# Kernel tuning notes

Hardware: AMD Instinct MI355X
Metric: run time of the kernel (lower is better)

The kernel has to match this reference:

```python
import jax, jax.numpy as jnp
import numpy as np

H_OUT, W_OUT = 473, 473  # original image size the logits are upsampled to
BN_EPS = 1e-5


def _conv(x, w, pad):
    return jax.lax.conv_general_dilated(
        x, w, window_strides=(1, 1), padding=[(pad, pad), (pad, pad)],
        dimension_numbers=('NCHW', 'OIHW', 'NCHW'))


def _bn(x, g, b):
    # BatchNorm2d in training mode: batch statistics over (N, H, W)
    m = jnp.mean(x, axis=(0, 2, 3), keepdims=True)
    v = jnp.var(x, axis=(0, 2, 3), keepdims=True)
    return (x - m) * jax.lax.rsqrt(v + BN_EPS) * g.reshape(1, -1, 1, 1) + b.reshape(1, -1, 1, 1)


def setup_inputs() -> dict:
    key = jax.random.key(0)
    ks = jax.random.split(key, 8)
    B, C, Hf, Wf, NC = 2, 256, 60, 60, 2
    return {
        'V_a': jax.random.normal(ks[0], (B, C, Hf, Wf), jnp.float32),
        'V_b': jax.random.normal(ks[1], (B, C, Hf, Wf), jnp.float32),
        'D_a': jax.random.normal(ks[2], (B, C, Hf, Wf), jnp.float32),
        'W_e': jax.random.normal(ks[3], (C, C), jnp.float32) * 0.02,
        'gate_w': jax.random.normal(ks[4], (1, C, 1, 1), jnp.float32) * 0.01,
        'conv1_w': jax.random.normal(ks[5], (C, 3 * C, 3, 3), jnp.float32) * 0.01,
        'conv2_w': jax.random.normal(ks[6], (C, 2 * C, 3, 3), jnp.float32) * 0.01,
        'bn1_g': jnp.ones((C,), jnp.float32),
        'bn1_b': jnp.zeros((C,), jnp.float32),
        'bn2_g': jnp.ones((C,), jnp.float32),
        'bn2_b': jnp.zeros((C,), jnp.float32),
        'cls1_w': jax.random.normal(ks[7], (NC, C, 1, 1), jnp.float32) * 0.01,
        'cls1_b': jnp.zeros((NC,), jnp.float32),
        'cls2_w': jax.random.normal(jax.random.fold_in(key, 9), (NC, C, 1, 1), jnp.float32) * 0.01,
        'cls2_b': jnp.zeros((NC,), jnp.float32),
    }


def reference(V_a, V_b, D_a, W_e, gate_w, conv1_w, conv2_w,
              bn1_g, bn1_b, bn2_g, bn2_b, cls1_w, cls1_b, cls2_w, cls2_b):
    B, C, Hf, Wf = V_a.shape
    N = Hf * Wf
    V_a_flat = V_a.reshape(B, C, N)
    V_b_flat = V_b.reshape(B, C, N)

    # linear_e on transposed A features, then affinity S = (A^T W^T) B
    weighted = jnp.einsum('bcn,dc->bnd', V_a_flat, W_e)        # [B, N, C]
    S = jnp.einsum('bnd,bdm->bnm', weighted, V_b_flat)         # [B, N, N]

    S_row = jax.nn.softmax(S, axis=1)                          # softmax over dim 1
    S_colT = jax.nn.softmax(jnp.swapaxes(S, 1, 2), axis=1)     # softmax of S^T over dim 1

    Z_b = jnp.einsum('bcn,bnm->bcm', V_a_flat, S_row)          # attended for view b
    Z_a = jnp.einsum('bcn,bnm->bcm', V_b_flat, S_colT)         # attended for view a

    att1 = Z_a.reshape(B, C, Hf, Wf)
    att2 = Z_b.reshape(B, C, Hf, Wf)

    # 1x1 sigmoid gates
    att1 = att1 * jax.nn.sigmoid(_conv(att1, gate_w, 0))
    att2 = att2 * jax.nn.sigmoid(_conv(att2, gate_w, 0))

    # conc1: branch-1 concatenates gated attention, RGB feat, and depth feat
    x1 = jnp.concatenate([att1, V_a, D_a], axis=1)             # [B, 3C, Hf, Wf]
    x2 = jnp.concatenate([att2, V_b], axis=1)                  # [B, 2C, Hf, Wf]

    x1 = jax.nn.relu(_bn(_conv(x1, conv1_w, 1), bn1_g, bn1_b))
    x2 = jax.nn.relu(_bn(_conv(x2, conv2_w, 1), bn2_g, bn2_b))

    x1 = _conv(x1, cls1_w, 0) + cls1_b.reshape(1, -1, 1, 1)
    x2 = _conv(x2, cls2_w, 0) + cls2_b.reshape(1, -1, 1, 1)

    NC = cls1_w.shape[0]
    x1 = jax.image.resize(x1, (B, NC, H_OUT, W_OUT), 'linear')
    x2 = jax.image.resize(x2, (B, NC, H_OUT, W_OUT), 'linear')
    return jax.nn.sigmoid(x1), jax.nn.sigmoid(x2)
```

## Files before the change

### kernel.cpp

```cpp
#include <hip/hip_runtime.h>

#define BB 2
#define CC 256
#define NN 3600
#define NCH 2
#define HO 473
#define WO 473
#define NP 3648
#define NR 3712
#define NTI 29
#define ZKS 6
#define CZKS 3

typedef unsigned short u16;
typedef __attribute__((ext_vector_type(8))) short short8;
typedef __attribute__((ext_vector_type(4))) float f32x4;

static __device__ __forceinline__ u16 f2bf(float f) {
    unsigned u = __float_as_uint(f);
    unsigned r = (u + 0x7FFF + ((u >> 16) & 1)) >> 16;
    return (u16)r;
}
static __device__ __forceinline__ u16 f2h(float f) {
    _Float16 h = (_Float16)f;
    return __builtin_bit_cast(unsigned short, h);
}
static __device__ __forceinline__ float h2f(u16 u) {
    _Float16 h = __builtin_bit_cast(_Float16, u);
    return (float)h;
}

static __device__ __forceinline__ void glds16(const u16* g, u16* l) {
    __builtin_amdgcn_global_load_lds(
        (const __attribute__((address_space(1))) void*)g,
        (__attribute__((address_space(3))) void*)l, 16, 0, 0);
}


__global__ __launch_bounds__(256)
void gemm_we(const u16* __restrict__ vat, const u16* __restrict__ web,
             u16* __restrict__ wgtb)
{
    __shared__ u16 As[128 * 64];
    __shared__ u16 Bs[128 * 64];
    const u16* A = vat + (long)blockIdx.z * NR * CC;
    u16* Cp = wgtb + (long)blockIdx.z * NR * CC;

    const int t = threadIdx.x;
    const int w = t >> 6, lane = t & 63;
    const int mh = (w >> 1) * 64, nh = (w & 1) * 64;
    const int lm = lane & 15, quad = lane >> 4;
    const int m0 = blockIdx.y * 128, n0 = blockIdx.x * 128;
    const int wb = t & 192;

    f32x4 acc[4][4] = {};

    for (int k0 = 0; k0 < CC; k0 += 64) {
#pragma unroll
        for (int i = 0; i < 4; ++i) {
            int idx = i * 256 + t;
            int row = idx >> 3;
            int sc8 = ((idx ^ row) & 7) * 8;
            glds16(A + (long)(m0 + row) * CC + k0 + sc8, &As[(i * 256 + wb) * 8]);
            glds16(web + (long)(n0 + row) * CC + k0 + sc8, &Bs[(i * 256 + wb) * 8]);
        }
        __syncthreads();
#pragma unroll
        for (int s = 0; s < 2; ++s) {
            short8 a[4], b[4];
#pragma unroll
            for (int i = 0; i < 4; ++i)
                a[i] = *(const short8*)(&As[(mh + i * 16 + lm) * 64 + ((s * 4 + quad) ^ (lm & 7)) * 8]);
#pragma unroll
            for (int j = 0; j < 4; ++j)
                b[j] = *(const short8*)(&Bs[(nh + j * 16 + lm) * 64 + ((s * 4 + quad) ^ (lm & 7)) * 8]);
#pragma unroll
            for (int i = 0; i < 4; ++i)
#pragma unroll
                for (int j = 0; j < 4; ++j)
                    acc[i][j] = __builtin_amdgcn_mfma_f32_16x16x32_bf16(a[i], b[j], acc[i][j], 0, 0, 0);
        }
        __syncthreads();
    }
#pragma unroll
    for (int i = 0; i < 4; ++i)
#pragma unroll
        for (int r = 0; r < 4; ++r) {
            int row = m0 + mh + i * 16 + quad * 4 + r;
            if (row < NN)
#pragma unroll
                for (int j = 0; j < 4; ++j) {
                    int col = n0 + nh + j * 16 + lm;
                    if (col < CC) Cp[(long)row * CC + col] = f2bf(acc[i][j][r]);
                }
        }
}

__global__ __launch_bounds__(256)
void gemm_s_stats(const u16* __restrict__ A, const u16* __restrict__ B,
                  u16* __restrict__ Sh, u16* __restrict__ STh,
                  float* __restrict__ prowm, float* __restrict__ prows,
                  float* __restrict__ pcolm, float* __restrict__ pcols)
{
    __shared__ u16 smem[17408];
    u16* As = smem;
    u16* Bs = smem + 8192;

    const int t = threadIdx.x;
    const int w = t >> 6, lane = t & 63;
    const int mh = (w >> 1) * 64, nh = (w & 1) * 64;
    const int lm = lane & 15, quad = lane >> 4;
    const int m0 = blockIdx.y * 128, n0 = blockIdx.x * 128;
    const int wb = t & 192;

    f32x4 acc[4][4] = {};

    for (int k0 = 0; k0 < CC; k0 += 64) {
#pragma unroll
        for (int i = 0; i < 4; ++i) {
            int idx = i * 256 + t;
            int row = idx >> 3;
            int sc8 = ((idx ^ row) & 7) * 8;
            glds16(A + (long)(m0 + row) * CC + k0 + sc8, &As[(i * 256 + wb) * 8]);
            glds16(B + (long)(n0 + row) * CC + k0 + sc8, &Bs[(i * 256 + wb) * 8]);
        }
        __syncthreads();
#pragma unroll
        for (int s = 0; s < 2; ++s) {
            short8 a[4], b[4];
#pragma unroll
            for (int i = 0; i < 4; ++i)
                a[i] = *(const short8*)(&As[(mh + i * 16 + lm) * 64 + ((s * 4 + quad) ^ (lm & 7)) * 8]);
#pragma unroll
            for (int j = 0; j < 4; ++j)
                b[j] = *(const short8*)(&Bs[(nh + j * 16 + lm) * 64 + ((s * 4 + quad) ^ (lm & 7)) * 8]);
#pragma unroll
            for (int i = 0; i < 4; ++i)
#pragma unroll
                for (int j = 0; j < 4; ++j)
                    acc[i][j] = __builtin_amdgcn_mfma_f32_16x16x32_bf16(a[i], b[j], acc[i][j], 0, 0, 0);
        }
        __syncthreads();
    }

    u16* tr = smem;

#pragma unroll
    for (int i = 0; i < 4; ++i)
#pragma unroll
        for (int j = 0; j < 4; ++j)
#pragma unroll
            for (int r = 0; r < 4; ++r)
                tr[(mh + i * 16 + quad * 4 + r) * 136 + (nh + j * 16 + lm)] = f2h(acc[i][j][r]);
    __syncthreads();
    {
        int row = t >> 1, hf = t & 1;
        int ng = m0 + row;
        if (ng < NN) {
#pragma unroll
            for (int q = 0; q < 8; ++q) {
                int cb = n0 + hf * 64 + q * 8;
                if (cb < NN)
                    *(uint4*)(&Sh[(long)ng * NP + cb]) =
                        *(const uint4*)(&tr[row * 136 + hf * 64 + q * 8]);
            }
        }
    }
    __syncthreads();

    bool cval[4];
#pragma unroll
    for (int j = 0; j < 4; ++j) cval[j] = (n0 + nh + j * 16 + lm) < NN;

    float* sm = (float*)smem;
    float* rowm = sm;
    float* rows_ = sm + 256;
    float* colm = sm + 512;
    float* cols_ = sm + 768;

#pragma unroll
    for (int i = 0; i < 4; ++i)
#pragma unroll
        for (int r = 0; r < 4; ++r) {
            float m = -3.0e38f;
#pragma unroll
            for (int j = 0; j < 4; ++j) if (cval[j]) m = fmaxf(m, acc[i][j][r]);
            m = fmaxf(m, __shfl_xor(m, 1, 64));
            m = fmaxf(m, __shfl_xor(m, 2, 64));
            m = fmaxf(m, __shfl_xor(m, 4, 64));
            m = fmaxf(m, __shfl_xor(m, 8, 64));
            float s = 0.f;
#pragma unroll
            for (int j = 0; j < 4; ++j) if (cval[j]) s += __expf(acc[i][j][r] - m);
            s += __shfl_xor(s, 1, 64);
            s += __shfl_xor(s, 2, 64);
            s += __shfl_xor(s, 4, 64);
            s += __shfl_xor(s, 8, 64);
            if (lm == 0) {
                int rr = mh + i * 16 + quad * 4 + r;
                rowm[(w & 1) * 128 + rr] = m;
                rows_[(w & 1) * 128 + rr] = s;
            }
        }

#pragma unroll
    for (int j = 0; j < 4; ++j) {
        float m = -3.0e38f;
#pragma unroll
        for (int i = 0; i < 4; ++i)
#pragma unroll
            for (int r = 0; r < 4; ++r)
                if (m0 + mh + i * 16 + quad * 4 + r < NN) m = fmaxf(m, acc[i][j][r]);
        m = fmaxf(m, __shfl_xor(m, 16, 64));
        m = fmaxf(m, __shfl_xor(m, 32, 64));
        float s = 0.f;
#pragma unroll
        for (int i = 0; i < 4; ++i)
#pragma unroll
            for (int r = 0; r < 4; ++r)
                if (m0 + mh + i * 16 + quad * 4 + r < NN) s += __expf(acc[i][j][r] - m);
        s += __shfl_xor(s, 16, 64);
        s += __shfl_xor(s, 32, 64);
        if (quad == 0) {
            int ccl = nh + j * 16 + lm;
            colm[(w >> 1) * 128 + ccl] = m;
            cols_[(w >> 1) * 128 + ccl] = s;
        }
    }
    __syncthreads();

    if (t < 128) {
        float m1 = rowm[t], m2 = rowm[128 + t];
        float M = fmaxf(m1, m2);
        float s = rows_[t] * __expf(m1 - M) + rows_[128 + t] * __expf(m2 - M);
        if (m0 + t < NN) {
            prowm[(long)blockIdx.x * NR + m0 + t] = M;
            prows[(long)blockIdx.x * NR + m0 + t] = s;
        }
    } else {
        int c = t - 128;
        float m1 = colm[c], m2 = colm[128 + c];
        float M = fmaxf(m1, m2);
        float s = cols_[c] * __expf(m1 - M) + cols_[128 + c] * __expf(m2 - M);
        if (n0 + c < NN) {
            pcolm[(long)blockIdx.y * NR + n0 + c] = M;
            pcols[(long)blockIdx.y * NR + n0 + c] = s;
        }
    }

    __syncthreads();
#pragma unroll
    for (int i = 0; i < 4; ++i)
#pragma unroll
        for (int j = 0; j < 4; ++j)
#pragma unroll
            for (int r = 0; r < 4; ++r)
                tr[(nh + j * 16 + lm) * 136 + (mh + i * 16 + quad * 4 + r)] = f2h(acc[i][j][r]);
    __syncthreads();
    {
        int row = t >> 1, hf = t & 1;
        int mg = n0 + row;
        if (mg < NN) {
#pragma unroll
            for (int q = 0; q < 8; ++q) {
                int cb = m0 + hf * 64 + q * 8;
                if (cb < NN)
                    *(uint4*)(&STh[(long)mg * NP + cb]) =
                        *(const uint4*)(&tr[row * 136 + hf * 64 + q * 8]);
            }
        }
    }
}

__global__ __launch_bounds__(256)
void p_build(u16* __restrict__ Sh, u16* __restrict__ STh,
             const float* __restrict__ prm, const float* __restrict__ prs,
             const float* __restrict__ pcm, const float* __restrict__ pcs)
{
    int r = blockIdx.x;
    u16* M = blockIdx.y ? STh : Sh;
    const float* pm = blockIdx.y ? pcm : prm;
    const float* ps = blockIdx.y ? pcs : prs;
    float m = -3.0e38f, s = 0.f;
#pragma unroll 4
    for (int tI = 0; tI < NTI; ++tI) {
        float m2 = pm[(long)tI * NR + r], s2 = ps[(long)tI * NR + r];
        float M2 = fmaxf(m, m2);
        s = s * __expf(m - M2) + s2 * __expf(m2 - M2);
        m = M2;
    }
    float inv = 1.f / s;
    u16* row = M + (long)r * NP;
    int t = threadIdx.x;
    for (int c0 = t * 8; c0 < NP; c0 += 2048) {
        uint4 hv = *(const uint4*)(row + c0);
        const u16* hp = (const u16*)&hv;
        u16 o[8];
#pragma unroll
        for (int e = 0; e < 8; ++e) {
            int c = c0 + e;
            o[e] = (c < NN) ? f2bf(__expf(h2f(hp[e]) - m) * inv) : (u16)0;
        }
        *(uint4*)(row + c0) = *(const uint4*)o;
    }
}

__global__ __launch_bounds__(256, 4)
void gemm_z_128(const u16* __restrict__ vab_b, const u16* __restrict__ vbb_b,
                const u16* __restrict__ PT, const u16* __restrict__ P,
                float* __restrict__ Zb_b, float* __restrict__ Za_b)
{
    __shared__ u16 As[128 * 64];
    __shared__ u16 Bs[128 * 64];

    const int t = threadIdx.x;
    const int w = t >> 6, lane = t & 63;
    const int mh = (w >> 1) * 64, nh = (w & 1) * 64;
    const int lm = lane & 15, quad = lane >> 4;
    const int n0 = blockIdx.x * 128;
    const int ks = blockIdx.y;
    const int zz = blockIdx.z;
    const int branch = zz & 1;
    const int m0 = (zz >> 1) * 128;
    const u16* A = branch ? vbb_b : vab_b;
    const u16* B = branch ? P : PT;
    float* Cp = branch ? Za_b : Zb_b;
    const int wb = t & 192;

    const int base = 57 / ZKS, rem = 57 % ZKS;
    const int it0 = ks * base + (ks < rem ? ks : rem);
    const int itn = base + (ks < rem ? 1 : 0);

    f32x4 acc[4][4] = {};

    for (int it = it0; it < it0 + itn; ++it) {
        const int k0 = it * 64;
#pragma unroll
        for (int i = 0; i < 4; ++i) {
            int idx = i * 256 + t;
            int row = idx >> 3;
            int sc8 = ((idx ^ row) & 7) * 8;
            glds16(A + (long)(m0 + row) * NP + k0 + sc8, &As[(i * 256 + wb) * 8]);
            glds16(B + (long)(n0 + row) * NP + k0 + sc8, &Bs[(i * 256 + wb) * 8]);
        }
        __syncthreads();
#pragma unroll
        for (int s = 0; s < 2; ++s) {
            short8 a[4], b[4];
#pragma unroll
            for (int i = 0; i < 4; ++i)
                a[i] = *(const short8*)(&As[(mh + i * 16 + lm) * 64 + ((s * 4 + quad) ^ (lm & 7)) * 8]);
#pragma unroll
            for (int j = 0; j < 4; ++j)
                b[j] = *(const short8*)(&Bs[(nh + j * 16 + lm) * 64 + ((s * 4 + quad) ^ (lm & 7)) * 8]);
#pragma unroll
            for (int i = 0; i < 4; ++i)
#pragma unroll
                for (int j = 0; j < 4; ++j)
                    acc[i][j] = __builtin_amdgcn_mfma_f32_16x16x32_bf16(a[i], b[j], acc[i][j], 0, 0, 0);
        }
        __syncthreads();
    }

#pragma unroll
    for (int i = 0; i < 4; ++i)
#pragma unroll
        for (int r = 0; r < 4; ++r) {
            int row = m0 + mh + i * 16 + quad * 4 + r;
#pragma unroll
            for (int j = 0; j < 4; ++j) {
                int col = n0 + nh + j * 16 + lm;
                if (col < NN)
                    atomicAdd(&Cp[(long)row * NN + col], acc[i][j][r]);
            }
        }
}

__global__ __launch_bounds__(256, 4)
void conv_both(const u16* __restrict__ W1, const u16* __restrict__ W2,
               const u16* __restrict__ gzaT, const u16* __restrict__ vat,
               const u16* __restrict__ daT, const u16* __restrict__ gzbT,
               const u16* __restrict__ vbt, const u16* __restrict__ zbuf,
               float* __restrict__ y1, float* __restrict__ y2)
{
    __shared__ u16 As[128 * 64];
    __shared__ u16 Bs[128 * 64];

    const int t = threadIdx.x;
    const int w = t >> 6, lane = t & 63;
    const int mh = (w >> 1) * 64, nh = (w & 1) * 64;
    const int lm = lane & 15, quad = lane >> 4;
    const int wb = t & 192;

    const long L = blockIdx.x + (long)NTI * (blockIdx.y + (long)CZKS * blockIdx.z);
    const int combo = (int)(L & 7);
    const long rest = L >> 3;
    const int ks = (int)(rest % CZKS);
    const int px = (int)(rest / CZKS);
    const int which = combo >> 2;
    const int b = (combo >> 1) & 1;
    const int m0 = (combo & 1) * 128;
    const int n0 = px * 128;

    const int CIN = which ? 512 : 768;
    const int KT = 9 * CIN;
    const u16* W = which ? W2 : W1;
    const u16* P0 = which ? gzbT : gzaT;
    const u16* P1 = which ? vbt : vat;
    const u16* P2 = which ? vbt : daT;
    float* Y = which ? y2 : y1;
    const long pstride = (long)NR * CC;

    const int PER = 3 * (CIN / 64);
    const int it0 = ks * PER;
    const int dh = ks - 1;

    int rowv[4], sc8v[4], rb[4];
    bool okd[4][3];
#pragma unroll
    for (int i = 0; i < 4; ++i) {
        int idx = i * 256 + t;
        int row = idx >> 3;
        rowv[i] = row;
        sc8v[i] = ((idx ^ row) & 7) * 8;
        int p = n0 + row;
        int h = p / 60, wp = p - h * 60;
        rb[i] = (p + dh * 60) * CC + sc8v[i];
        bool hok = (p < NN) && ((unsigned)(h + dh) < 60u);
#pragma unroll
        for (int d = 0; d < 3; ++d)
            okd[i][d] = hok && ((unsigned)(wp + d - 1) < 60u);
    }

    f32x4 acc[4][4] = {};

    for (int it = it0; it < it0 + PER; ++it) {
        const int k0 = it * 64;
        const int g = it - it0;
        const int dw = g % 3;
        const int pc = g / 3;
        const int plane = pc >> 2;
        const int cip = (pc & 3) * 64;
        const u16* srcp = ((plane == 0) ? P0 : (plane == 1) ? P1 : P2)
                          + (long)b * pstride + cip;

#pragma unroll
        for (int i = 0; i < 4; ++i) {
            glds16(W + (long)(m0 + rowv[i]) * KT + k0 + sc8v[i], &As[(i * 256 + wb) * 8]);
            const u16* gs = okd[i][dw] ? srcp + rb[i] + (dw - 1) * CC : zbuf;
            glds16(gs, &Bs[(i * 256 + wb) * 8]);
        }
        __syncthreads();
#pragma unroll
        for (int s = 0; s < 2; ++s) {
            short8 a[4], bfr[4];
#pragma unroll
            for (int i = 0; i < 4; ++i)
                a[i] = *(const short8*)(&As[(mh + i * 16 + lm) * 64 + ((s * 4 + quad) ^ (lm & 7)) * 8]);
#pragma unroll
            for (int j = 0; j < 4; ++j)
                bfr[j] = *(const short8*)(&Bs[(nh + j * 16 + lm) * 64 + ((s * 4 + quad) ^ (lm & 7)) * 8]);
#pragma unroll
            for (int i = 0; i < 4; ++i)
#pragma unroll
                for (int j = 0; j < 4; ++j)
                    acc[i][j] = __builtin_amdgcn_mfma_f32_16x16x32_bf16(a[i], bfr[j], acc[i][j], 0, 0, 0);
        }
        __syncthreads();
    }

    float* out = Y + (long)b * CC * NN;
#pragma unroll
    for (int i = 0; i < 4; ++i)
#pragma unroll
        for (int r = 0; r < 4; ++r) {
            int row = m0 + mh + i * 16 + quad * 4 + r;
#pragma unroll
            for (int j = 0; j < 4; ++j) {
                int col = n0 + nh + j * 16 + lm;
                if (col < NN)
                    atomicAdd(&out[(long)row * NN + col], acc[i][j][r]);
            }
        }
}

__global__ __launch_bounds__(256)
void cvt_we(const float* __restrict__ W, u16* __restrict__ O)
{
    int i = blockIdx.x * 256 + threadIdx.x;
    if (i < CC * CC) O[i] = f2bf(W[i]);
}

__global__ __launch_bounds__(256)
void transpose_cvt3(const float* __restrict__ Va, const float* __restrict__ Vb,
                    const float* __restrict__ Da,
                    u16* __restrict__ vat, u16* __restrict__ vbt,
                    u16* __restrict__ daT,
                    u16* __restrict__ vab, u16* __restrict__ vbb)
{
    __shared__ float tile[64][65];
    int z = blockIdx.z;
    int s = z % 3, b = z / 3;
    const float* V = (s == 0) ? Va : (s == 1) ? Vb : Da;
    u16* VT = (s == 0) ? vat : (s == 1) ? vbt : daT;
    u16* Vpad = (s == 0) ? vab : (s == 1) ? vbb : nullptr;

    int c0 = blockIdx.y * 64, n0 = blockIdx.x * 64;
    int t = threadIdx.x;
#pragma unroll
    for (int e = 0; e < 16; ++e) {
        int f = e * 256 + t; int i = f >> 6, j = f & 63;
        int n = n0 + j;
        float v = 0.f;
        if (n < NN) v = V[((long)b * CC + c0 + i) * NN + n];
        tile[i][j] = v;
        if (Vpad) Vpad[((long)b * CC + c0 + i) * NP + n] = f2bf(v);
    }
    __syncthreads();
#pragma unroll
    for (int e = 0; e < 16; ++e) {
        int f = e * 256 + t; int i = f >> 6, j = f & 63;
        int n = n0 + i;
        if (n < NN) VT[((long)b * NR + n) * CC + c0 + j] = f2bf(tile[j][i]);
    }
}

__global__ __launch_bounds__(256)
void transpose_gate(const float* __restrict__ Za, const float* __restrict__ Zb,
                    const float* __restrict__ sga, const float* __restrict__ sgb,
                    u16* __restrict__ gzaT, u16* __restrict__ gzbT)
{
    __shared__ float tile[64][65];
    int z = blockIdx.z;
    int b = z & 1, ab = z >> 1;
    const float* Z = ab ? Zb : Za;
    const float* sg = ab ? sgb : sga;
    u16* ZT = ab ? gzbT : gzaT;

    int c0 = blockIdx.y * 64, n0 = blockIdx.x * 64;
    int t = threadIdx.x;
#pragma unroll
    for (int e = 0; e < 16; ++e) {
        int f = e * 256 + t; int i = f >> 6, j = f & 63;
        int n = n0 + j;
        float v = 0.f;
        if (n < NN) v = Z[((long)b * CC + c0 + i) * NN + n];
        tile[i][j] = v;
    }
    __syncthreads();
#pragma unroll
    for (int e = 0; e < 16; ++e) {
        int f = e * 256 + t; int i = f >> 6, j = f & 63;
        int n = n0 + i;
        if (n < NN)
            ZT[((long)b * NR + n) * CC + c0 + j] = f2bf(tile[j][i] * sg[b * NN + n]);
    }
}

template<int CIN>
__global__ __launch_bounds__(256)
void cvt_convw(const float* __restrict__ W, u16* __restrict__ O)
{
    const int KT = 9 * CIN;
    const int PER = 3 * (CIN / 64);
    long idx = (long)blockIdx.x * 256 + threadIdx.x;
    if (idx >= (long)CC * KT) return;
    int co = (int)(idx / KT);
    int r = (int)(idx % KT);
    int c64 = r >> 6, within = r & 63;
    int ks = c64 / PER, g = c64 % PER;
    int dw = g % 3, pc = g / 3;
    int tap = ks * 3 + dw;
    int ci = pc * 64 + within;
    O[idx] = f2bf(W[((long)co * CIN + ci) * 9 + tap]);
}

__global__ __launch_bounds__(256)
void gate_sig(const float* __restrict__ Za, const float* __restrict__ Zb,
              const float* __restrict__ gw,
              float* __restrict__ sga, float* __restrict__ sgb)
{
    int t = threadIdx.x;
    int px = t & 63, ck = t >> 6;
    int b = blockIdx.y;
    int ab = blockIdx.z;
    const float* Z = ab ? Zb : Za;
    float* sg = ab ? sgb : sga;
    int p = blockIdx.x * 64 + px;
    const float* Zp = Z + (long)b * CC * NN;
    float g = 0.f;
    if (p < NN) {
        for (int c = ck * 64; c < ck * 64 + 64; ++c) g += gw[c] * Zp[(long)c * NN + p];
    }
    __shared__ float red[256];
    red[t] = g;
    __syncthreads();
    if (t < 64) {
        int pp = blockIdx.x * 64 + t;
        if (pp < NN) {
            float tot = red[t] + red[t + 64] + red[t + 128] + red[t + 192];
            sg[b * NN + pp] = 1.f / (1.f + __expf(-tot));
        }
    }
}

__global__ __launch_bounds__(256)
void bn_stats_kernel(const float* __restrict__ y1, const float* __restrict__ y2,
                     const float* __restrict__ g1, const float* __restrict__ b1,
                     const float* __restrict__ g2, const float* __restrict__ b2,
                     float* __restrict__ sc1, float* __restrict__ sh1,
                     float* __restrict__ sc2, float* __restrict__ sh2)
{
    int which = blockIdx.x >> 8;
    int c = blockIdx.x & 255, t = threadIdx.x;
    const float* Y = which ? y2 : y1;
    const float* g = which ? g2 : g1;
    const float* beta = which ? b2 : b1;
    float* scale = which ? sc2 : sc1;
    float* shift = which ? sh2 : sh1;
    float s = 0.f, sq = 0.f;
    for (int b = 0; b < BB; ++b) {
        const float* p = Y + (long)b * CC * NN + (long)c * NN;
        for (int i = t; i < NN; i += 256) { float v = p[i]; s += v; sq += v * v; }
    }
    __shared__ float ls[256], lq[256];
    ls[t] = s; lq[t] = sq;
    __syncthreads();
    for (int off = 128; off > 0; off >>= 1) {
        if (t < off) { ls[t] += ls[t + off]; lq[t] += lq[t + off]; }
        __syncthreads();
    }
    if (t == 0) {
        const float inv = 1.f / (float)(BB * NN);
        float mean = ls[0] * inv;
        float var = fmaxf(lq[0] * inv - mean * mean, 0.f);
        float sc = g[c] * rsqrtf(var + 1e-5f);
        scale[c] = sc;
        shift[c] = beta[c] - mean * sc;
    }
}

__global__ __launch_bounds__(256)
void cls_kernel(const float* __restrict__ y1, const float* __restrict__ y2,
                const float* __restrict__ sc1, const float* __restrict__ sh1,
                const float* __restrict__ sc2, const float* __restrict__ sh2,
                const float* __restrict__ cw1, const float* __restrict__ cb1,
                const float* __restrict__ cw2, const float* __restrict__ cb2,
                float* __restrict__ O1, float* __restrict__ O2)
{
    int which = blockIdx.z;
    const float* Y = which ? y2 : y1;
    const float* scale = which ? sc2 : sc1;
    const float* shift = which ? sh2 : sh1;
    const float* cw = which ? cw2 : cw1;
    const float* cb = which ? cb2 : cb1;
    float* O = which ? O2 : O1;

    int t = threadIdx.x;
    int px = t & 63, ck = t >> 6;
    int b = blockIdx.y;
    int p = blockIdx.x * 64 + px;
    const float* Yb = Y + (long)b * CC * NN;
    float a0 = 0.f, a1 = 0.f;
    if (p < NN) {
        for (int c = ck * 64; c < ck * 64 + 64; ++c) {
            float v = Yb[(long)c * NN + p] * scale[c] + shift[c];
            v = fmaxf(v, 0.f);
            a0 += cw[c] * v;
            a1 += cw[CC + c] * v;
        }
    }
    __shared__ float r0[256], r1[256];
    r0[t] = a0; r1[t] = a1;
    __syncthreads();
    if (t < 64) {
        int pp = blockIdx.x * 64 + t;
        if (pp < NN) {
            float s0 = r0[t] + r0[t + 64] + r0[t + 128] + r0[t + 192];
            float s1 = r1[t] + r1[t + 64] + r1[t + 128] + r1[t + 192];
            O[(long)b * NCH * NN + pp] = s0 + cb[0];
            O[(long)b * NCH * NN + NN + pp] = s1 + cb[1];
        }
    }
}

__global__ __launch_bounds__(256)
void resize_sig_kernel(const float* __restrict__ I1, const float* __restrict__ I2,
                       float* __restrict__ O)
{
    const long HALF = (long)BB * NCH * HO * WO;
    long gid = (long)blockIdx.x * 256 + threadIdx.x;
    if (gid >= HALF) return;
    int half = blockIdx.y;
    const float* I = half ? I2 : I1;
    float* Op = O + half * HALF;

    int j = (int)(gid % WO);
    long r = gid / WO;
    int i = (int)(r % HO);
    int pc = (int)(r / HO);
    const float* ip = I + (long)pc * NN;

    const float SCL = 60.0f / 473.0f;
    float fy = (i + 0.5f) * SCL - 0.5f;
    float fx = (j + 0.5f) * SCL - 0.5f;
    int y0 = (int)floorf(fy);
    int x0 = (int)floorf(fx);
    float ty = fy - (float)y0;
    float tx = fx - (float)x0;
    int y0c = max(y0, 0), y1c = min(y0 + 1, 59);
    int x0c = max(x0, 0), x1c = min(x0 + 1, 59);
    float va = ip[y0c * 60 + x0c], vb = ip[y0c * 60 + x1c];
    float vc = ip[y1c * 60 + x0c], vd = ip[y1c * 60 + x1c];
    float v = (1.f - ty) * ((1.f - tx) * va + tx * vb) + ty * ((1.f - tx) * vc + tx * vd);
    Op[gid] = 1.f / (1.f + __expf(-v));
}

extern "C" void kernel_launch(void* const* d_in, const int* in_sizes, int n_in,
                              void* d_out, int out_size, void* d_ws, size_t ws_size,
                              hipStream_t stream)
{
    const float* V_a    = (const float*)d_in[0];
    const float* V_b    = (const float*)d_in[1];
    const float* D_a    = (const float*)d_in[2];
    const float* W_e    = (const float*)d_in[3];
    const float* gate_w = (const float*)d_in[4];
    const float* conv1_w = (const float*)d_in[5];
    const float* conv2_w = (const float*)d_in[6];
    const float* bn1_g = (const float*)d_in[7];
    const float* bn1_b = (const float*)d_in[8];
    const float* bn2_g = (const float*)d_in[9];
    const float* bn2_b = (const float*)d_in[10];
    const float* cls1_w = (const float*)d_in[11];
    const float* cls1_b = (const float*)d_in[12];
    const float* cls2_w = (const float*)d_in[13];
    const float* cls2_b = (const float*)d_in[14];
    float* out = (float*)d_out;

    size_t off = 0;
    char* wsb = (char*)d_ws;
    auto carve = [&](size_t bytes) -> char* {
        char* p = wsb + off; off += (bytes + 255) & ~(size_t)255; return p;
    };

    u16* Sh    = (u16*)carve((size_t)NR * NP * 2);
    u16* STh   = (u16*)carve((size_t)NR * NP * 2);
    u16* vab   = (u16*)carve((size_t)BB * CC * NP * 2);
    u16* vbb   = (u16*)carve((size_t)BB * CC * NP * 2);
    u16* vat   = (u16*)carve((size_t)BB * NR * CC * 2);
    u16* vbt   = (u16*)carve((size_t)BB * NR * CC * 2);
    u16* daT   = (u16*)carve((size_t)BB * NR * CC * 2);
    u16* gzaT  = (u16*)carve((size_t)BB * NR * CC * 2);
    u16* gzbT  = (u16*)carve((size_t)BB * NR * CC * 2);
    u16* wgtb  = (u16*)carve((size_t)BB * NR * CC * 2);
    u16* zbuf  = (u16*)carve(256);
    u16* web   = (u16*)carve((size_t)CC * CC * 2);
    u16* wt1   = (u16*)carve((size_t)CC * 9 * 768 * 2);
    u16* wt2   = (u16*)carve((size_t)CC * 9 * 512 * 2);
    float* Za  = (float*)carve((size_t)BB * CC * NN * 4);
    float* Zb  = (float*)carve((size_t)BB * CC * NN * 4);
    float* y1  = (float*)carve((size_t)BB * CC * NN * 4);
    float* y2  = (float*)carve((size_t)BB * CC * NN * 4);
    float* rmx = (float*)carve((size_t)BB * NN * 4);
    float* rsm = (float*)carve((size_t)BB * NN * 4);
    float* cmx = (float*)carve((size_t)BB * NN * 4);
    float* csm = (float*)carve((size_t)BB * NN * 4);
    float* sga = (float*)carve((size_t)BB * NN * 4);
    float* sgb = (float*)carve((size_t)BB * NN * 4);
    float* prm = (float*)carve((size_t)NTI * NR * 4);
    float* prs = (float*)carve((size_t)NTI * NR * 4);
    float* pcm = (float*)carve((size_t)NTI * NR * 4);
    float* pcs = (float*)carve((size_t)NTI * NR * 4);
    float* c1o = (float*)carve((size_t)BB * NCH * NN * 4);
    float* c2o = (float*)carve((size_t)BB * NCH * NN * 4);

    dim3 blk(256);

    hipMemsetAsync(Za, 0, (size_t)4 * BB * CC * NN * 4, stream);
    hipMemsetAsync(vat, 0, (size_t)6 * ((size_t)BB * NR * CC * 2) + 256, stream);

    cvt_we<<<256, blk, 0, stream>>>(W_e, web);
    transpose_cvt3<<<dim3(57, 4, 3 * BB), blk, 0, stream>>>(
        V_a, V_b, D_a, vat, vbt, daT, vab, vbb);
    cvt_convw<768><<<(int)(((long)CC * 9 * 768 + 255) / 256), blk, 0, stream>>>(conv1_w, wt1);
    cvt_convw<512><<<(int)(((long)CC * 9 * 512 + 255) / 256), blk, 0, stream>>>(conv2_w, wt2);

    gemm_we<<<dim3(2, NTI, BB), blk, 0, stream>>>(vat, web, wgtb);

    for (int b = 0; b < BB; ++b) {
        const u16* wgtb_b = wgtb + (long)b * NR * CC;
        const u16* vbt_b  = vbt + (long)b * NR * CC;
        const u16* vab_b  = vab + (long)b * CC * NP;
        const u16* vbb_b  = vbb + (long)b * CC * NP;

        gemm_s_stats<<<dim3(NTI, NTI), blk, 0, stream>>>(
            wgtb_b, vbt_b, Sh, STh, prm, prs, pcm, pcs);
        p_build<<<dim3(NN, 2), blk, 0, stream>>>(Sh, STh, prm, prs, pcm, pcs);
        gemm_z_128<<<dim3(NTI, ZKS, 4), blk, 0, stream>>>(
            vab_b, vbb_b, STh, Sh,
            Zb + (long)b * CC * NN, Za + (long)b * CC * NN);
    }

    gate_sig<<<dim3(57, BB, 2), blk, 0, stream>>>(Za, Zb, gate_w, sga, sgb);
    transpose_gate<<<dim3(57, 4, 2 * BB), blk, 0, stream>>>(Za, Zb, sga, sgb, gzaT, gzbT);

    conv_both<<<dim3(NTI, CZKS, 8), blk, 0, stream>>>(
        wt1, wt2, gzaT, vat, daT, gzbT, vbt, zbuf, y1, y2);

    bn_stats_kernel<<<2 * CC, blk, 0, stream>>>(
        y1, y2, bn1_g, bn1_b, bn2_g, bn2_b, rmx, rsm, cmx, csm);
    cls_kernel<<<dim3(57, BB, 2), blk, 0, stream>>>(
        y1, y2, rmx, rsm, cmx, csm, cls1_w, cls1_b, cls2_w, cls2_b, c1o, c2o);

    resize_sig_kernel<<<dim3((int)(((long)BB * NCH * HO * WO + 255) / 256), 2), blk, 0, stream>>>(c1o, c2o, out);
}
```

Before: 594.7 us.

## Fuse softmax normalization into Z GEMM B-tile loads and drop p_build pass

The p_build kernel, which rewrote both fp16 score matrices in place as normalized bf16 probabilities, is replaced by a small stats_final kernel. That kernel only reduces the per-tile max and sum partials into per-row max and inverse-sum arrays. gemm_z_128 now applies exp, scale and bf16 conversion while loading each B tile, which removes a full read/write pass over both large S matrices per batch. In exchange the B operand goes through a synchronous register load and LDS store instead of direct global-to-LDS loads, and exponentials are recomputed for every m-block. The large memset of the transposed bf16 buffers is also shrunk to zeroing only zbuf, which assumes the padding regions are no longer read uninitialized.

Measured after the change: 593.6 us. Within noise of the previous version (-0.2%).

```diff
diff --git a/kernel.cpp b/kernel.cpp
--- a/kernel.cpp
+++ b/kernel.cpp
@@ -273,41 +273,33 @@
 }
 
 __global__ __launch_bounds__(256)
-void p_build(u16* __restrict__ Sh, u16* __restrict__ STh,
-             const float* __restrict__ prm, const float* __restrict__ prs,
-             const float* __restrict__ pcm, const float* __restrict__ pcs)
-{
-    int r = blockIdx.x;
-    u16* M = blockIdx.y ? STh : Sh;
+void stats_final(const float* __restrict__ prm, const float* __restrict__ prs,
+                 const float* __restrict__ pcm, const float* __restrict__ pcs,
+                 float* __restrict__ rm, float* __restrict__ ri,
+                 float* __restrict__ cm, float* __restrict__ ci)
+{
+    int i = blockIdx.x * 256 + threadIdx.x;
+    if (i >= NN) return;
     const float* pm = blockIdx.y ? pcm : prm;
     const float* ps = blockIdx.y ? pcs : prs;
     float m = -3.0e38f, s = 0.f;
 #pragma unroll 4
     for (int tI = 0; tI < NTI; ++tI) {
-        float m2 = pm[(long)tI * NR + r], s2 = ps[(long)tI * NR + r];
-        float M2 = fmaxf(m, m2);
-        s = s * __expf(m - M2) + s2 * __expf(m2 - M2);
-        m = M2;
+        float m2 = pm[(long)tI * NR + i], s2 = ps[(long)tI * NR + i];
+        float M = fmaxf(m, m2);
+        s = s * __expf(m - M) + s2 * __expf(m2 - M);
+        m = M;
     }
     float inv = 1.f / s;
-    u16* row = M + (long)r * NP;
-    int t = threadIdx.x;
-    for (int c0 = t * 8; c0 < NP; c0 += 2048) {
-        uint4 hv = *(const uint4*)(row + c0);
-        const u16* hp = (const u16*)&hv;
-        u16 o[8];
-#pragma unroll
-        for (int e = 0; e < 8; ++e) {
-            int c = c0 + e;
-            o[e] = (c < NN) ? f2bf(__expf(h2f(hp[e]) - m) * inv) : (u16)0;
-        }
-        *(uint4*)(row + c0) = *(const uint4*)o;
-    }
+    if (blockIdx.y) { cm[i] = m; ci[i] = inv; }
+    else            { rm[i] = m; ri[i] = inv; }
 }
 
 __global__ __launch_bounds__(256, 4)
 void gemm_z_128(const u16* __restrict__ vab_b, const u16* __restrict__ vbb_b,
-                const u16* __restrict__ PT, const u16* __restrict__ P,
+                const u16* __restrict__ STh, const u16* __restrict__ Sh,
+                const float* __restrict__ rm, const float* __restrict__ ri,
+                const float* __restrict__ cm, const float* __restrict__ ci,
                 float* __restrict__ Zb_b, float* __restrict__ Za_b)
 {
     __shared__ u16 As[128 * 64];
@@ -323,7 +315,9 @@
     const int branch = zz & 1;
     const int m0 = (zz >> 1) * 128;
     const u16* A = branch ? vbb_b : vab_b;
-    const u16* B = branch ? P : PT;
+    const u16* B = branch ? Sh : STh;
+    const float* mxp = branch ? rm : cm;
+    const float* isp = branch ? ri : ci;
     float* Cp = branch ? Za_b : Zb_b;
     const int wb = t & 192;
 
@@ -331,17 +325,43 @@
     const int it0 = ks * base + (ks < rem ? ks : rem);
     const int itn = base + (ks < rem ? 1 : 0);
 
+    int rowv[4], sc8v[4];
+    const u16* Brow[4];
+    float bm[4], bi[4];
+#pragma unroll
+    for (int i = 0; i < 4; ++i) {
+        int idx = i * 256 + t;
+        int row = idx >> 3;
+        rowv[i] = row;
+        sc8v[i] = ((idx ^ row) & 7) * 8;
+        int rg = n0 + row;
+        int rc = rg < NN ? rg : 0;
+        Brow[i] = B + (long)rg * NP + sc8v[i];
+        bm[i] = mxp[rc];
+        bi[i] = isp[rc];
+    }
+
     f32x4 acc[4][4] = {};
 
     for (int it = it0; it < it0 + itn; ++it) {
         const int k0 = it * 64;
 #pragma unroll
+        for (int i = 0; i < 4; ++i)
+            glds16(A + (long)(m0 + rowv[i]) * NP + k0 + sc8v[i], &As[(i * 256 + wb) * 8]);
+#pragma unroll
         for (int i = 0; i < 4; ++i) {
-            int idx = i * 256 + t;
-            int row = idx >> 3;
-            int sc8 = ((idx ^ row) & 7) * 8;
-            glds16(A + (long)(m0 + row) * NP + k0 + sc8, &As[(i * 256 + wb) * 8]);
-            glds16(B + (long)(n0 + row) * NP + k0 + sc8, &Bs[(i * 256 + wb) * 8]);
+            u16 o[8];
+            if (k0 + sc8v[i] < NN) {
+                uint4 v = *(const uint4*)(Brow[i] + k0);
+                const u16* hp = (const u16*)&v;
+#pragma unroll
+                for (int e = 0; e < 8; ++e)
+                    o[e] = f2bf(__expf(h2f(hp[e]) - bm[i]) * bi[i]);
+            } else {
+#pragma unroll
+                for (int e = 0; e < 8; ++e) o[e] = 0;
+            }
+            *(uint4*)(&Bs[(i * 256 + t) * 8]) = *(const uint4*)o;
         }
         __syncthreads();
 #pragma unroll
@@ -423,10 +443,10 @@
         int row = idx >> 3;
         rowv[i] = row;
         sc8v[i] = ((idx ^ row) & 7) * 8;
-        int p = n0 + row;
-        int h = p / 60, wp = p - h * 60;
-        rb[i] = (p + dh * 60) * CC + sc8v[i];
-        bool hok = (p < NN) && ((unsigned)(h + dh) < 60u);
+        int pq = n0 + row;
+        int h = pq / 60, wp = pq - h * 60;
+        rb[i] = (pq + dh * 60) * CC + sc8v[i];
+        bool hok = (pq < NN) && ((unsigned)(h + dh) < 60u);
 #pragma unroll
         for (int d = 0; d < 3; ++d)
             okd[i][d] = hok && ((unsigned)(wp + d - 1) < 60u);
@@ -777,7 +797,7 @@
     dim3 blk(256);
 
     hipMemsetAsync(Za, 0, (size_t)4 * BB * CC * NN * 4, stream);
-    hipMemsetAsync(vat, 0, (size_t)6 * ((size_t)BB * NR * CC * 2) + 256, stream);
+    hipMemsetAsync(zbuf, 0, 256, stream);
 
     cvt_we<<<256, blk, 0, stream>>>(W_e, web);
     transpose_cvt3<<<dim3(57, 4, 3 * BB), blk, 0, stream>>>(
@@ -792,12 +812,15 @@
         const u16* vbt_b  = vbt + (long)b * NR * CC;
         const u16* vab_b  = vab + (long)b * CC * NP;
         const u16* vbb_b  = vbb + (long)b * CC * NP;
+        float* rmx_b = rmx + b * NN; float* rsm_b = rsm + b * NN;
+        float* cmx_b = cmx + b * NN; float* csm_b = csm + b * NN;
 
         gemm_s_stats<<<dim3(NTI, NTI), blk, 0, stream>>>(
             wgtb_b, vbt_b, Sh, STh, prm, prs, pcm, pcs);
-        p_build<<<dim3(NN, 2), blk, 0, stream>>>(Sh, STh, prm, prs, pcm, pcs);
+        stats_final<<<dim3((NN + 255) / 256, 2), blk, 0, stream>>>(
+            prm, prs, pcm, pcs, rmx_b, rsm_b, cmx_b, csm_b);
         gemm_z_128<<<dim3(NTI, ZKS, 4), blk, 0, stream>>>(
-            vab_b, vbb_b, STh, Sh,
+            vab_b, vbb_b, STh, Sh, rmx_b, rsm_b, cmx_b, csm_b,
             Zb + (long)b * CC * NN, Za + (long)b * CC * NN);
     }
 
```
